# Optimization experiments

Measured on AMD Instinct MI355X. Metric: run time of the kernel, lower is better.

The kernel has to match this reference:

```python
import jax, jax.numpy as jnp
import numpy as np

B, T, H, HY, E, L = 32, 256, 1024, 256, 64, 2


def setup_inputs() -> dict:
    key = jax.random.key(0)
    ks = jax.random.split(key, 16)
    rn = lambda k, s, sc=0.05: jax.random.normal(k, s, dtype=jnp.float32) * sc
    return {
        'input': rn(ks[0], (B, T, H), 1.0),
        'w_ih': rn(ks[1], (L, 4 * H, H)),
        'w_hh': rn(ks[2], (L, 4 * H, H)),
        'hyper_w_ih': rn(ks[3], (L, 4 * HY, 2 * H)),
        'hyper_w_hh': rn(ks[4], (L, 4 * HY, HY)),
        'hyper_b': rn(ks[5], (L, 4 * HY)),
        'w_zh': rn(ks[6], (L, 4 * E, HY)),
        'b_zh': jnp.ones((L, 4 * E), jnp.float32),
        'w_zx': rn(ks[7], (L, 4 * E, HY)),
        'b_zx': jnp.ones((L, 4 * E), jnp.float32),
        'w_zb': rn(ks[8], (L, 4 * E, HY)),
        'w_dh': rn(ks[9], (L, 4, H, E), 1.0 / E),
        'w_dx': rn(ks[10], (L, 4, H, E), 1.0 / E),
        'w_db': rn(ks[11], (L, 4, H, E)),
        'b0': rn(ks[12], (L, 4 * H)),
    }


def reference(input, w_ih, w_hh, hyper_w_ih, hyper_w_hh, hyper_b,
              w_zh, b_zh, w_zx, b_zx, w_zb, w_dh, w_dx, w_db, b0):
    L = w_ih.shape[0]
    Bb = input.shape[0]
    Hh = w_hh.shape[-1]
    Hy = hyper_w_hh.shape[-1]
    Ee = w_dh.shape[-1]

    def cell(l, xt, h, c, hh, hc):
        # hyper (meta) LSTM step: input is concat(x, h_main)
        xh = jnp.concatenate([xt, h], axis=-1)
        hg = xh @ hyper_w_ih[l].T + hh @ hyper_w_hh[l].T + hyper_b[l]
        hi, hf, hgc, ho = jnp.split(hg, 4, axis=-1)
        hc2 = jax.nn.sigmoid(hf) * hc + jax.nn.sigmoid(hi) * jnp.tanh(hgc)
        hh2 = jax.nn.sigmoid(ho) * jnp.tanh(hc2)
        # gate-wise embeddings z (B, 4, E) then project to per-gate scale vectors (B, 4H)
        zh = (hh2 @ w_zh[l].T + b_zh[l]).reshape(Bb, 4, Ee)
        zx = (hh2 @ w_zx[l].T + b_zx[l]).reshape(Bb, 4, Ee)
        zb = (hh2 @ w_zb[l].T).reshape(Bb, 4, Ee)
        dh = jnp.einsum('bge,ghe->bgh', zh, w_dh[l]).reshape(Bb, 4 * Hh)
        dx = jnp.einsum('bge,ghe->bgh', zx, w_dx[l]).reshape(Bb, 4 * Hh)
        db = jnp.einsum('bge,ghe->bgh', zb, w_db[l]).reshape(Bb, 4 * Hh) + b0[l]
        # main LSTM gates, dynamically scaled by hypernetwork
        pre = dh * (h @ w_hh[l].T) + dx * (xt @ w_ih[l].T) + db
        i, f, g, o = jnp.split(pre, 4, axis=-1)
        c2 = jax.nn.sigmoid(f) * c + jax.nn.sigmoid(i) * jnp.tanh(g)
        h2 = jax.nn.sigmoid(o) * jnp.tanh(c2)
        return h2, c2, hh2, hc2

    def step(carry, xt):
        h, c, hh, hc = carry  # each (L, B, .)
        hs, cs, hhs, hcs = [], [], [], []
        inp = xt
        for l in range(L):
            h2, c2, hh2, hc2 = cell(l, inp, h[l], c[l], hh[l], hc[l])
            inp = h2
            hs.append(h2); cs.append(c2); hhs.append(hh2); hcs.append(hc2)
        carry = (jnp.stack(hs), jnp.stack(cs), jnp.stack(hhs), jnp.stack(hcs))
        return carry, inp  # top-layer hidden

    init = (jnp.zeros((L, Bb, Hh), input.dtype), jnp.zeros((L, Bb, Hh), input.dtype),
            jnp.zeros((L, Bb, Hy), input.dtype), jnp.zeros((L, Bb, Hy), input.dtype))
    carry, ys = jax.lax.scan(step, init, jnp.swapaxes(input, 0, 1))
    h_seq = jnp.swapaxes(ys, 0, 1)  # (B, T, H)
    return h_seq, carry[0][-1], carry[1][-1]
```

## Files before the change

### kernel.cpp

```cpp
#include <hip/hip_runtime.h>

typedef __bf16 bf16;
typedef __bf16 bf16x8 __attribute__((ext_vector_type(8)));
typedef __bf16 bf16x4 __attribute__((ext_vector_type(4)));
typedef float f32x4 __attribute__((ext_vector_type(4)));
typedef unsigned long long u64;

#define SCOPE_AGENT __HIP_MEMORY_SCOPE_AGENT


__device__ __forceinline__ float sigf(float x) { return 1.0f / (1.0f + __expf(-x)); }
__device__ __forceinline__ float tanhf_fast(float x) {
  float e = __expf(-2.0f * fabsf(x));
  float r = (1.0f - e) / (1.0f + e);
  return copysignf(r, x);
}
__device__ __forceinline__ f32x4 mfma16(bf16x8 a, bf16x8 b, f32x4 c) {
  return __builtin_amdgcn_mfma_f32_16x16x32_bf16(a, b, c, 0, 0, 0);
}
__device__ __forceinline__ u64 uld(const u64* p) { return __hip_atomic_load(p, __ATOMIC_RELAXED, SCOPE_AGENT); }
__device__ __forceinline__ void ust(u64* p, u64 v) { __hip_atomic_store(p, v, __ATOMIC_RELAXED, SCOPE_AGENT); }
__device__ __forceinline__ int ildi(const int* p) { return __hip_atomic_load(p, __ATOMIC_RELAXED, SCOPE_AGENT); }
__device__ __forceinline__ void isti(int* p, int v) { __hip_atomic_store(p, v, __ATOMIC_RELAXED, SCOPE_AGENT); }
__device__ __forceinline__ void fstf(float* p, float v) { __hip_atomic_store(p, v, __ATOMIC_RELAXED, SCOPE_AGENT); }
__device__ __forceinline__ void usti32(unsigned* p, unsigned v) { __hip_atomic_store(p, v, __ATOMIC_RELAXED, SCOPE_AGENT); }

__global__ void detect_kernel(const void* probe, int* flag) {
  __shared__ int cnt;
  if (threadIdx.x == 0) cnt = 0;
  __syncthreads();
  const bf16* p = (const bf16*)probe;
  int local = 0;
  for (int j = threadIdx.x; j < 8192; j += 256) {
    float x = (float)p[j];
    bool wild = (x != x) || (fabsf(x) > 1e3f) || (x != 0.0f && fabsf(x) < 1e-30f);
    local += wild ? 1 : 0;
  }
  atomicAdd(&cnt, local);
  __syncthreads();
  if (threadIdx.x == 0) *flag = (cnt > 64) ? 1 : 0;
}

struct CvtSrc { const void* s[15]; };
struct CvtDst { bf16* d[15]; };

__global__ __launch_bounds__(256) void convert_kernel(CvtSrc S, CvtDst D, const int* flag) {
  const int pre[16] = {0, 8388608, 16777216, 25165824, 29360128, 29884416, 29886464,
                       30017536, 30018048, 30149120, 30149632, 30280704, 30804992,
                       31329280, 31853568, 31861760};
  const int fp32 = *flag;
  const int nvec = 31861760 / 4;
  for (int v = blockIdx.x * 256 + threadIdx.x; v < nvec; v += gridDim.x * 256) {
    int e = v * 4;
    int seg = 0;
#pragma unroll
    for (int k = 1; k < 15; ++k) seg += (e >= pre[k]) ? 1 : 0;
    int off = e - pre[seg];
    bf16* d = D.d[seg] + off;
    if (fp32) {
      const float* s = (const float*)S.s[seg] + off;
      float4 x = *(const float4*)s;
      d[0] = (bf16)x.x; d[1] = (bf16)x.y; d[2] = (bf16)x.z; d[3] = (bf16)x.w;
    } else {
      const bf16* s = (const bf16*)S.s[seg] + off;
      d[0] = s[0]; d[1] = s[1]; d[2] = s[2]; d[3] = s[3];
    }
  }
}

__global__ void init_kernel(u64* zbase) {
  int i = blockIdx.x * 256 + threadIdx.x;
  zbase[i] = 0ull;
}

__global__ __launch_bounds__(256) void gemm_pre(
    const bf16* __restrict__ A, const bf16* __restrict__ w_ih_l,
    const bf16* __restrict__ hwih_l, bf16* __restrict__ Xp, float* __restrict__ Hxp) {
  constexpr int LDT = 72;
  __shared__ alignas(16) bf16 As[64 * LDT];
  __shared__ alignas(16) bf16 Bs[64 * LDT];
  const int bm = blockIdx.x & 127;
  const int bn = blockIdx.x >> 7;
  const int m0 = bm * 64, n0 = bn * 64;
  const int tid = threadIdx.x;
  const int lane = tid & 63, wid = tid >> 6;
  const int l15 = lane & 15, q = lane >> 4;
  const int srow = tid >> 2, sk = (tid & 3) * 16;
  const bf16* arow = A + (size_t)(m0 + srow) * 1024;
  const int n = n0 + srow;
  const bf16* brow = (n < 4096) ? (w_ih_l + (size_t)n * 1024)
                                : (hwih_l + (size_t)(n - 4096) * 2048);
  f32x4 acc[4] = {};
  for (int kb = 0; kb < 1024; kb += 64) {
    *(bf16x8*)(&As[srow * LDT + sk])     = *(const bf16x8*)(arow + kb + sk);
    *(bf16x8*)(&As[srow * LDT + sk + 8]) = *(const bf16x8*)(arow + kb + sk + 8);
    *(bf16x8*)(&Bs[srow * LDT + sk])     = *(const bf16x8*)(brow + kb + sk);
    *(bf16x8*)(&Bs[srow * LDT + sk + 8]) = *(const bf16x8*)(brow + kb + sk + 8);
    __syncthreads();
#pragma unroll
    for (int kk = 0; kk < 64; kk += 32) {
      bf16x8 av = *(const bf16x8*)(&As[(wid * 16 + l15) * LDT + kk + q * 8]);
#pragma unroll
      for (int j = 0; j < 4; ++j) {
        bf16x8 bv = *(const bf16x8*)(&Bs[(j * 16 + l15) * LDT + kk + q * 8]);
        acc[j] = mfma16(av, bv, acc[j]);
      }
    }
    __syncthreads();
  }
#pragma unroll
  for (int j = 0; j < 4; ++j) {
    const int gn = n0 + j * 16 + l15;
#pragma unroll
    for (int r = 0; r < 4; ++r) {
      const int gm = m0 + wid * 16 + q * 4 + r;
      float v = acc[j][r];
      if (gn < 4096) Xp[(size_t)gm * 4096 + gn] = (bf16)v;
      else           Hxp[(size_t)gm * 1024 + (gn - 4096)] = v;
    }
  }
}

struct SeqArgs {
  const bf16 *w_hh, *hwih, *hwhh, *hyb;
  const bf16 *w_zh, *b_zh, *w_zx, *b_zx, *w_zb;
  const bf16 *w_dh, *w_dx, *w_db, *b0;
  const bf16 *Xp; const float *Hxp;
  const bf16 *w_ih1;
  bf16 *Xp1c; float *Hxp1c;
  u64 *Y0;
  u64 *hpub;
  u64 *hh2pub;
  float *outp;
  int *flags;
};

__global__ __launch_bounds__(256) void seq_kernel(SeqArgs a) {
  __shared__ char smem[41472] __attribute__((aligned(16)));
  bf16 (*hstage)[1032] = (bf16(*)[1032])smem;
  bf16 (*hhK)[264]    = (bf16(*)[264])(smem + 33024);
  float* hgL          = (float*)(smem + 33024);
  bf16 (*hA4)[1032]   = (bf16(*)[1032])smem;
  bf16 (*hh2A)[264]   = (bf16(*)[264])(smem + 8256);
  float (*RhL)[256]   = (float(*)[256])(smem + 10368);
  float (*zsL)[768]   = (float(*)[768])(smem + 14464);
  float (*presL)[256] = (float(*)[256])(smem + 26752);
  bf16 (*hbuf)[64]    = (bf16(*)[64])(smem + 30848);
  bf16*  As = (bf16*)smem;
  bf16*  Bs = (bf16*)(smem + 9216);
  float* Ct = (float*)(smem + 18432);

  const int tid = threadIdx.x;
  const int lane = tid & 63, wid = tid >> 6;
  const int l15 = lane & 15, q = lane >> 4;
  const int blk = blockIdx.x;
  const int xcd = blk & 7, slot = blk >> 3;
  const int layer = xcd >> 2, xl = xcd & 3;
  const int s16 = xl * 4 + (slot & 3);
  const int bq = slot >> 2;
  const int lblk = bq * 16 + s16;
  const int hd = s16 >> 1;
  const int mh = (bq == hd) ? 0 : ((bq == ((hd + 4) & 7)) ? 1 : -1);
  const bool isHyper = (((s16 & 1) == 0) && (mh >= 0));
  const int myMh = bq >> 2;

  u64* hbase  = a.hpub + (size_t)layer * 16384;
  u64* h2base = a.hh2pub + (size_t)layer * 4096;
  int* gchunkp= a.flags + 32;
  int* arrp   = a.flags + 64 + layer * 2048;
  int* arrp0  = a.flags + 64;
  int* hh2fp  = a.flags + 4160 + layer * 256;
  int* carrp  = a.flags + 4672;

  const bf16* whh_l = a.w_hh + (size_t)layer * 4194304;
  const bf16* hybl  = a.hyb + layer * 1024;
  const bf16* bzh_l = a.b_zh + layer * 256;
  const bf16* bzx_l = a.b_zx + layer * 256;
  const bf16* b0_l  = a.b0 + (size_t)layer * 4096;
  const int cb = tid >> 6, chl = tid & 63;

  float c_reg = 0.0f;
  float hc[2] = {0, 0};

  const bf16* zrow[12];
#pragma unroll
  for (int j = 0; j < 12; ++j) {
    int ng = wid * 12 + j, tau = ng >> 4;
    const bf16* base = (tau == 0) ? a.w_zh : (tau == 1) ? a.w_zx : a.w_zb;
    zrow[j] = base + ((size_t)layer * 256 + (ng & 15) * 16 + l15) * 256;
  }
  const bf16* rrow[4];
#pragma unroll
  for (int nt = 0; nt < 4; ++nt)
    rrow[nt] = whh_l + (size_t)(wid * 1024 + s16 * 64 + nt * 16 + l15) * 1024;
  const bf16* hirow[2];
  const bf16* hhrow[2];
#pragma unroll
  for (int nt = 0; nt < 2; ++nt) {
    const int row = wid * 256 + hd * 32 + nt * 16 + l15;
    hirow[nt] = a.hwih + (size_t)layer * 2097152 + (size_t)row * 2048 + 1024;
    hhrow[nt] = a.hwhh + (size_t)layer * 262144 + (size_t)row * 256;
  }
  const size_t wdo = ((size_t)(layer * 4 + wid) * 1024 + s16 * 64 + lane) * 64;
  const bf16 *pdh = a.w_dh + wdo, *pdx = a.w_dx + wdo, *pdb = a.w_db + wdo;

  for (int t = 0; t < 256; ++t) {
    const int tloc = t & 31;
    u64* wslot = hbase + (size_t)(t & 1) * 8192;
    const u64* rslot = hbase + (size_t)((t + 1) & 1) * 8192;
    u64* wcur = h2base + (size_t)(t & 1) * 2048;
    const u64* rK = h2base + (size_t)((t + 1) & 1) * 2048;

    if (layer == 1 && tloc == 0) {
      const int k = t >> 5;
      if (tid < 128) {
        while (ildi(arrp0 + tid * 16) < (k + 1) * 32) __builtin_amdgcn_s_sleep(2);
      } else if (t > 0) {
        while (ildi(arrp + (tid - 128) * 16) < t) __builtin_amdgcn_s_sleep(2);
      }
      __atomic_signal_fence(__ATOMIC_SEQ_CST);
      __syncthreads();
      const int srow = tid >> 2, sk = (tid & 3) * 16;
      for (int tt = 0; tt < 10; ++tt) {
        const int tile = lblk * 10 + tt;
        const int m0 = (tile & 15) * 64, n0 = (tile >> 4) * 64;
        const int m = m0 + srow;
        const u64* arow = a.Y0 + (((size_t)(m >> 5) * 256 + k * 32 + (m & 31)) << 8);
        const int n = n0 + srow;
        const bf16* brow = (n < 4096) ? (a.w_ih1 + (size_t)n * 1024)
                                      : (a.hwih + 2097152 + (size_t)(n - 4096) * 2048);
        f32x4 acc[4] = {};
        for (int kb = 0; kb < 1024; kb += 64) {
          const int c0 = (kb + sk) >> 2;
          u64 a0 = uld(arow + c0),     a1 = uld(arow + c0 + 1);
          u64 a2 = uld(arow + c0 + 2), a3 = uld(arow + c0 + 3);
          *(u64*)&As[srow * 72 + sk]      = a0;
          *(u64*)&As[srow * 72 + sk + 4]  = a1;
          *(u64*)&As[srow * 72 + sk + 8]  = a2;
          *(u64*)&As[srow * 72 + sk + 12] = a3;
          *(bf16x8*)&Bs[srow * 72 + sk]     = *(const bf16x8*)(brow + kb + sk);
          *(bf16x8*)&Bs[srow * 72 + sk + 8] = *(const bf16x8*)(brow + kb + sk + 8);
          __syncthreads();
#pragma unroll
          for (int kk = 0; kk < 64; kk += 32) {
            bf16x8 av = *(const bf16x8*)&As[(wid * 16 + l15) * 72 + kk + q * 8];
#pragma unroll
            for (int j = 0; j < 4; ++j) {
              bf16x8 bv = *(const bf16x8*)&Bs[(j * 16 + l15) * 72 + kk + q * 8];
              acc[j] = mfma16(av, bv, acc[j]);
            }
          }
          __syncthreads();
        }
#pragma unroll
        for (int j = 0; j < 4; ++j)
#pragma unroll
          for (int r = 0; r < 4; ++r)
            Ct[(wid * 16 + q * 4 + r) * 64 + j * 16 + l15] = acc[j][r];
        __syncthreads();
#pragma unroll
        for (int e = 0; e < 4; ++e) {
          const int qd = tid * 4 + e;
          const int row = qd >> 4, col4 = (qd & 15) * 4;
          f32x4 v = *(const f32x4*)&Ct[row * 64 + col4];
          const int gm = m0 + row, gn = n0 + col4;
          if (gn < 4096) {
            union { bf16 h[4]; u64 u; } pk;
#pragma unroll
            for (int x = 0; x < 4; ++x) pk.h[x] = (bf16)v[x];
            ust((u64*)a.Xp1c + ((((size_t)gm << 12) + gn) >> 2), pk.u);
          } else {
            float* hp = a.Hxp1c + ((size_t)gm << 10) + (gn - 4096);
#pragma unroll
            for (int x = 0; x < 4; ++x) fstf(hp + x, v[x]);
          }
        }
        __syncthreads();
      }
      __atomic_signal_fence(__ATOMIC_SEQ_CST);
      __builtin_amdgcn_s_waitcnt(0);
      __syncthreads();
      if (tid == 0) isti(carrp + lblk * 16, k + 1);
      if (lblk == 0 && wid == 0) {
        for (;;) {
          int v0 = ildi(carrp + lane * 32);
          int v1 = ildi(carrp + lane * 32 + 16);
          if (__all((v0 >= k + 1) && (v1 >= k + 1))) break;
          __builtin_amdgcn_s_sleep(2);
        }
        __atomic_signal_fence(__ATOMIC_SEQ_CST);
        if (lane == 0) isti(gchunkp, k + 1);
      }
      if (tid == 0) { while (ildi(gchunkp) < k + 1) __builtin_amdgcn_s_sleep(2); }
      __atomic_signal_fence(__ATOMIC_SEQ_CST);
      __syncthreads();
    }

    if (t > 0) {
      if (tid < 16) {
        while (ildi(arrp + (bq * 16 + tid) * 16) < t) __builtin_amdgcn_s_sleep(1);
      }
      if (isHyper) {
        if (tid >= 64 && tid < 128) {
          const int j = tid - 64;
          const int fl = (mh * 4 + (j >> 4)) * 16 + (j & 15);
          while (ildi(arrp + fl * 16) < t) __builtin_amdgcn_s_sleep(1);
        }
        if (tid >= 128 && tid < 136) {
          while (ildi(hh2fp + ((tid - 128) * 2 + mh) * 16) < t) __builtin_amdgcn_s_sleep(1);
        }
      }
    }
    __atomic_signal_fence(__ATOMIC_SEQ_CST);
    __syncthreads();

    if (isHyper) {
      for (int i = tid; i < 4096; i += 256) {
        int b = i >> 8, u = i & 255;
        *(u64*)&hstage[b][u * 4] = uld(rslot + ((size_t)(mh * 16 + b) << 8) + u);
      }
      for (int i = tid; i < 1024; i += 256) {
        int b = i >> 6, u = i & 63;
        *(u64*)&hhK[b][u * 4] = uld(rK + ((size_t)(mh * 16 + b) << 6) + u);
      }
      __syncthreads();
      f32x4 acc[2] = {};
      for (int kk = 0; kk < 1024; kk += 32) {
        int ko = kk + q * 8;
        bf16x8 a0 = *(const bf16x8*)&hstage[l15][ko];
#pragma unroll
        for (int nt = 0; nt < 2; ++nt) {
          bf16x8 bv = *(const bf16x8*)(hirow[nt] + ko);
          acc[nt] = mfma16(a0, bv, acc[nt]);
        }
      }
      for (int kk = 0; kk < 256; kk += 32) {
        int ko = kk + q * 8;
        bf16x8 a0 = *(const bf16x8*)&hhK[l15][ko];
#pragma unroll
        for (int nt = 0; nt < 2; ++nt) {
          bf16x8 bv = *(const bf16x8*)(hhrow[nt] + ko);
          acc[nt] = mfma16(a0, bv, acc[nt]);
        }
      }
      __syncthreads();
#pragma unroll
      for (int nt = 0; nt < 2; ++nt)
#pragma unroll
        for (int r = 0; r < 4; ++r)
          hgL[(wid * 16 + q * 4 + r) * 32 + nt * 16 + l15] = acc[nt][r];
      __syncthreads();
      {
        const int b16 = tid >> 4, d0 = (tid & 15) * 2;
        const int b = mh * 16 + b16;
        float hx2[4][2];
        if (layer == 0) {
          const float* hx = a.Hxp + ((size_t)b * 256 + t) * 1024 + hd * 32 + d0;
#pragma unroll
          for (int g = 0; g < 4; ++g) {
            hx2[g][0] = hx[g * 256]; hx2[g][1] = hx[g * 256 + 1];
          }
        } else {
          const u64* hx1 = (const u64*)a.Hxp1c + (((size_t)b * 32 + tloc) << 9)
                         + ((hd * 32 + d0) >> 1);
#pragma unroll
          for (int g = 0; g < 4; ++g) {
            u64 w = uld(hx1 + g * 128);
            hx2[g][0] = __uint_as_float((unsigned)(w & 0xffffffffu));
            hx2[g][1] = __uint_as_float((unsigned)(w >> 32));
          }
        }
        union { bf16 h[2]; unsigned u; } pk;
#pragma unroll
        for (int dd = 0; dd < 2; ++dd) {
          int d = d0 + dd, gd = hd * 32 + d;
          float hi  = hgL[(0 * 16 + b16) * 32 + d] + (float)hybl[gd]       + hx2[0][dd];
          float hf  = hgL[(1 * 16 + b16) * 32 + d] + (float)hybl[256 + gd] + hx2[1][dd];
          float hgv = hgL[(2 * 16 + b16) * 32 + d] + (float)hybl[512 + gd] + hx2[2][dd];
          float ho  = hgL[(3 * 16 + b16) * 32 + d] + (float)hybl[768 + gd] + hx2[3][dd];
          hc[dd] = sigf(hf) * hc[dd] + sigf(hi) * tanhf_fast(hgv);
          pk.h[dd] = (bf16)(sigf(ho) * tanhf_fast(hc[dd]));
        }
        usti32((unsigned*)wcur + b * 128 + hd * 16 + (d0 >> 1), pk.u);
      }
      __atomic_signal_fence(__ATOMIC_SEQ_CST);
      __builtin_amdgcn_s_waitcnt(0);
      __syncthreads();
      if (tid == 0) isti(hh2fp + (hd * 2 + mh) * 16, t + 1);
    }
    __syncthreads();

    for (int i = tid; i < 1024; i += 256) {
      int b = i >> 8, u = i & 255;
      *(u64*)&hA4[b][u * 4] = uld(rslot + ((size_t)(bq * 4 + b) << 8) + u);
    }
    __syncthreads();
    {
      f32x4 racc[4] = {};
      for (int kk = 0; kk < 1024; kk += 32) {
        const int ko = kk + q * 8;
        bf16x8 av = *(const bf16x8*)&hA4[l15 & 3][ko];
#pragma unroll
        for (int nt = 0; nt < 4; ++nt) {
          bf16x8 bv = *(const bf16x8*)(rrow[nt] + ko);
          racc[nt] = mfma16(av, bv, racc[nt]);
        }
      }
      if (lane < 16) {
#pragma unroll
        for (int nt = 0; nt < 4; ++nt)
#pragma unroll
          for (int r = 0; r < 4; ++r)
            RhL[r][wid * 64 + nt * 16 + lane] = racc[nt][r];
      }
    }
    if (tid < 8) {
      while (ildi(hh2fp + (tid * 2 + myMh) * 16) < t + 1) __builtin_amdgcn_s_sleep(1);
    }
    __atomic_signal_fence(__ATOMIC_SEQ_CST);
    __syncthreads();
    {
      int b = tid >> 6, u = tid & 63;
      *(u64*)&hh2A[b][u * 4] = uld(wcur + ((size_t)(bq * 4 + b) << 6) + u);
    }
    __syncthreads();
    {
      f32x4 zacc[12] = {};
      for (int kk = 0; kk < 256; kk += 32) {
        const int ko = kk + q * 8;
        bf16x8 av = *(const bf16x8*)&hh2A[l15 & 3][ko];
#pragma unroll
        for (int j = 0; j < 12; ++j) {
          bf16x8 bv = *(const bf16x8*)(zrow[j] + ko);
          zacc[j] = mfma16(av, bv, zacc[j]);
        }
      }
      if (lane < 16) {
#pragma unroll
        for (int j = 0; j < 12; ++j) {
          int ng = wid * 12 + j, tau = ng >> 4, col = (ng & 15) * 16 + lane;
          float bias = (tau == 0) ? (float)bzh_l[col] : (tau == 1) ? (float)bzx_l[col] : 0.0f;
#pragma unroll
          for (int r = 0; r < 4; ++r) zsL[r][tau * 256 + col] = zacc[j][r] + bias;
        }
      }
    }
    __syncthreads();
    {
      float dH[4] = {}, dX[4] = {}, dB[4] = {};
      for (int e0 = 0; e0 < 64; e0 += 4) {
        bf16x4 wh = *(const bf16x4*)(pdh + e0);
        bf16x4 wx = *(const bf16x4*)(pdx + e0);
        bf16x4 wb = *(const bf16x4*)(pdb + e0);
        f32x4 zh_[4], zx_[4], zb_[4];
#pragma unroll
        for (int b = 0; b < 4; ++b) {
          zh_[b] = *(const f32x4*)&zsL[b][wid * 64 + e0];
          zx_[b] = *(const f32x4*)&zsL[b][256 + wid * 64 + e0];
          zb_[b] = *(const f32x4*)&zsL[b][512 + wid * 64 + e0];
        }
#pragma unroll
        for (int jj = 0; jj < 4; ++jj) {
          float whf = (float)wh[jj], wxf = (float)wx[jj], wbf = (float)wb[jj];
#pragma unroll
          for (int b = 0; b < 4; ++b) {
            dH[b] += zh_[b][jj] * whf;
            dX[b] += zx_[b][jj] * wxf;
            dB[b] += zb_[b][jj] * wbf;
          }
        }
      }
      const int n = wid * 1024 + s16 * 64 + lane;
#pragma unroll
      for (int b = 0; b < 4; ++b) {
        float rh = RhL[b][wid * 64 + lane];
        float xp;
        if (layer == 0) {
          xp = (float)a.Xp[((size_t)(bq * 4 + b) * 256 + t) * 4096 + n];
        } else {
          u64 w = uld((const u64*)a.Xp1c
                      + ((((size_t)((bq * 4 + b) * 32 + tloc) << 12) + (n & ~3)) >> 2));
          xp = __uint_as_float(((unsigned)(w >> ((n & 3) * 16)) & 0xffffu) << 16);
        }
        float b0v = (float)b0_l[n];
        presL[b][wid * 64 + lane] = dH[b] * rh + dX[b] * xp + dB[b] + b0v;
      }
    }
    __syncthreads();
    {
      float iv = presL[cb][chl];
      float fv = presL[cb][64 + chl];
      float gv = presL[cb][128 + chl];
      float ov = presL[cb][192 + chl];
      c_reg = sigf(fv) * c_reg + sigf(iv) * tanhf_fast(gv);
      float hn = sigf(ov) * tanhf_fast(c_reg);
      hbuf[cb][chl] = (bf16)hn;
      if (layer) {
        const size_t oo = ((size_t)(bq * 4 + cb) * 256 + t) * 1024 + s16 * 64 + chl;
        a.outp[oo] = hn;
        if (t == 255) {
          a.outp[8388608 + (bq * 4 + cb) * 1024 + s16 * 64 + chl] = hn;
          a.outp[8421376 + (bq * 4 + cb) * 1024 + s16 * 64 + chl] = c_reg;
        }
      }
    }
    __syncthreads();
    if (tid < 64) {
      int b = tid >> 4, u = tid & 15;
      u64 pk = *(const u64*)&hbuf[b][u * 4];
      ust(wslot + ((size_t)(bq * 4 + b) << 8) + s16 * 16 + u, pk);
      if (layer == 0)
        ust(a.Y0 + (((size_t)(bq * 4 + b) * 256 + t) << 8) + s16 * 16 + u, pk);
    }
    __atomic_signal_fence(__ATOMIC_SEQ_CST);
    __builtin_amdgcn_s_waitcnt(0);
    __syncthreads();
    if (tid == 0) isti(arrp + lblk * 16, t + 1);
  }
}

extern "C" void kernel_launch(void* const* d_in, const int* in_sizes, int n_in,
                              void* d_out, int out_size, void* d_ws, size_t ws_size,
                              hipStream_t stream) {
  float* outp = (float*)d_out;
  char* ws = (char*)d_ws;
  bf16*  Xp     = (bf16*) (ws);
  float* Hxp    = (float*)(ws + 67108864ull);
  u64*   Y0     = (u64*)  (ws + 100663296ull);
  bf16* c_input = (bf16*)(ws + 117669888ull);
  bf16*  Xp1c   = c_input;
  float* Hxp1c  = (float*)(ws + 117669888ull + 8388608ull);
  bf16* c_w_ih  = (bf16*)(ws + 134447104ull);
  bf16* c_w_hh  = (bf16*)(ws + 151224320ull);
  bf16* c_hwih  = (bf16*)(ws + 168001536ull);
  bf16* c_hwhh  = (bf16*)(ws + 176390144ull);
  bf16* c_hyb   = (bf16*)(ws + 177438720ull);
  bf16* c_wzh   = (bf16*)(ws + 177442816ull);
  bf16* c_bzh   = (bf16*)(ws + 177704960ull);
  bf16* c_wzx   = (bf16*)(ws + 177705984ull);
  bf16* c_bzx   = (bf16*)(ws + 177968128ull);
  bf16* c_wzb   = (bf16*)(ws + 177969152ull);
  bf16* c_wdh   = (bf16*)(ws + 178231296ull);
  bf16* c_wdx   = (bf16*)(ws + 179279872ull);
  bf16* c_wdb   = (bf16*)(ws + 180328448ull);
  bf16* c_b0    = (bf16*)(ws + 181377024ull);
  int*  dflag   = (int*) (ws + 181393408ull);
  char* pubb    = ws + 181397504ull;
  u64*   hpub   = (u64*)  (pubb + 0);
  u64*   hh2pub = (u64*)  (pubb + 262144);
  int*   flags  = (int*)  (pubb + 327680);

  hipLaunchKernelGGL(detect_kernel, dim3(1), dim3(256), 0, stream, d_in[2], dflag);
  CvtSrc S; CvtDst D;
  for (int i = 0; i < 15; ++i) S.s[i] = d_in[i];
  D.d[0] = c_input; D.d[1] = c_w_ih; D.d[2] = c_w_hh; D.d[3] = c_hwih; D.d[4] = c_hwhh;
  D.d[5] = c_hyb;   D.d[6] = c_wzh;  D.d[7] = c_bzh;  D.d[8] = c_wzx;  D.d[9] = c_bzx;
  D.d[10] = c_wzb;  D.d[11] = c_wdh; D.d[12] = c_wdx; D.d[13] = c_wdb; D.d[14] = c_b0;
  hipLaunchKernelGGL(convert_kernel, dim3(2048), dim3(256), 0, stream, S, D, dflag);

  hipLaunchKernelGGL(init_kernel, dim3(176), dim3(256), 0, stream, (u64*)pubb);
  hipLaunchKernelGGL(gemm_pre, dim3(10240), dim3(256), 0, stream,
                     c_input, c_w_ih, c_hwih, Xp, Hxp);

  SeqArgs sa;
  sa.w_hh = c_w_hh; sa.hwih = c_hwih; sa.hwhh = c_hwhh; sa.hyb = c_hyb;
  sa.w_zh = c_wzh; sa.b_zh = c_bzh; sa.w_zx = c_wzx; sa.b_zx = c_bzx; sa.w_zb = c_wzb;
  sa.w_dh = c_wdh; sa.w_dx = c_wdx; sa.w_db = c_wdb; sa.b0 = c_b0;
  sa.Xp = Xp; sa.Hxp = Hxp;
  sa.w_ih1 = c_w_ih + (size_t)4194304;
  sa.Xp1c = Xp1c; sa.Hxp1c = Hxp1c;
  sa.Y0 = Y0;
  sa.hpub = hpub; sa.hh2pub = hh2pub;
  sa.outp = outp;
  sa.flags = flags;
  hipLaunchKernelGGL(seq_kernel, dim3(256), dim3(256), 0, stream, sa);
}
```

Before: 20.41 ms.

## Redistribute hyper-LSTM work so each batch group computes its own hyper step

The hyper LSTM step moves off the 16 dedicated blocks that each handled 16 batches by 32 hidden units, each waiting on many producer flags. It now runs on 4 blocks per batch quad (sq==0), each covering 4 batches by 64 units. Those blocks reuse the main-path h staging buffer hA4, so they no longer stage a separate 16-row h tile, and synchronization shrinks to per-quad flags. The aim is shorter cross-block dependency chains and less redundant staging per step. In exchange, the MFMA A operand uses only 4 of its 16 rows, so more weight bandwidth is spent per useful output.

```diff
diff --git a/kernel.cpp b/kernel.cpp
--- a/kernel.cpp
+++ b/kernel.cpp
@@ -23,7 +23,7 @@
 __device__ __forceinline__ int ildi(const int* p) { return __hip_atomic_load(p, __ATOMIC_RELAXED, SCOPE_AGENT); }
 __device__ __forceinline__ void isti(int* p, int v) { __hip_atomic_store(p, v, __ATOMIC_RELAXED, SCOPE_AGENT); }
 __device__ __forceinline__ void fstf(float* p, float v) { __hip_atomic_store(p, v, __ATOMIC_RELAXED, SCOPE_AGENT); }
-__device__ __forceinline__ void usti32(unsigned* p, unsigned v) { __hip_atomic_store(p, v, __ATOMIC_RELAXED, SCOPE_AGENT); }
+__device__ __forceinline__ float fldf(const float* p) { return __hip_atomic_load(p, __ATOMIC_RELAXED, SCOPE_AGENT); }
 
 __global__ void detect_kernel(const void* probe, int* flag) {
   __shared__ int cnt;
@@ -136,16 +136,16 @@
 };
 
 __global__ __launch_bounds__(256) void seq_kernel(SeqArgs a) {
-  __shared__ char smem[41472] __attribute__((aligned(16)));
-  bf16 (*hstage)[1032] = (bf16(*)[1032])smem;
-  bf16 (*hhK)[264]    = (bf16(*)[264])(smem + 33024);
-  float* hgL          = (float*)(smem + 33024);
+  __shared__ char smem[38144] __attribute__((aligned(16)));
   bf16 (*hA4)[1032]   = (bf16(*)[1032])smem;
-  bf16 (*hh2A)[264]   = (bf16(*)[264])(smem + 8256);
-  float (*RhL)[256]   = (float(*)[256])(smem + 10368);
-  float (*zsL)[768]   = (float(*)[768])(smem + 14464);
-  float (*presL)[256] = (float(*)[256])(smem + 26752);
-  bf16 (*hbuf)[64]    = (bf16(*)[64])(smem + 30848);
+  bf16 (*hhPrev)[264] = (bf16(*)[264])(smem + 8256);
+  bf16 (*hh2A)[264]   = (bf16(*)[264])(smem + 10368);
+  float (*RhL)[256]   = (float(*)[256])(smem + 12480);
+  float (*zsL)[768]   = (float(*)[768])(smem + 16576);
+  float (*presL)[256] = (float(*)[256])(smem + 28864);
+  bf16 (*hbuf)[64]    = (bf16(*)[64])(smem + 32960);
+  float* hgS          = (float*)(smem + 33472);
+  bf16*  hh2own       = (bf16*)(smem + 37568);
   bf16*  As = (bf16*)smem;
   bf16*  Bs = (bf16*)(smem + 9216);
   float* Ct = (float*)(smem + 18432);
@@ -156,21 +156,18 @@
   const int blk = blockIdx.x;
   const int xcd = blk & 7, slot = blk >> 3;
   const int layer = xcd >> 2, xl = xcd & 3;
-  const int s16 = xl * 4 + (slot & 3);
-  const int bq = slot >> 2;
+  const int bq = slot >> 2, sq = slot & 3;
+  const int s16 = sq * 4 + xl;
   const int lblk = bq * 16 + s16;
-  const int hd = s16 >> 1;
-  const int mh = (bq == hd) ? 0 : ((bq == ((hd + 4) & 7)) ? 1 : -1);
-  const bool isHyper = (((s16 & 1) == 0) && (mh >= 0));
-  const int myMh = bq >> 2;
+  const bool isHyper = (sq == 0);
 
   u64* hbase  = a.hpub + (size_t)layer * 16384;
   u64* h2base = a.hh2pub + (size_t)layer * 4096;
   int* gchunkp= a.flags + 32;
   int* arrp   = a.flags + 64 + layer * 2048;
   int* arrp0  = a.flags + 64;
-  int* hh2fp  = a.flags + 4160 + layer * 256;
-  int* carrp  = a.flags + 4672;
+  int* hh2fp  = a.flags + 4608 + layer * 512;
+  int* carrp  = a.flags + 5632;
 
   const bf16* whh_l = a.w_hh + (size_t)layer * 4194304;
   const bf16* hybl  = a.hyb + layer * 1024;
@@ -180,7 +177,7 @@
   const int cb = tid >> 6, chl = tid & 63;
 
   float c_reg = 0.0f;
-  float hc[2] = {0, 0};
+  float hc = 0.0f;
 
   const bf16* zrow[12];
 #pragma unroll
@@ -193,14 +190,9 @@
 #pragma unroll
   for (int nt = 0; nt < 4; ++nt)
     rrow[nt] = whh_l + (size_t)(wid * 1024 + s16 * 64 + nt * 16 + l15) * 1024;
-  const bf16* hirow[2];
-  const bf16* hhrow[2];
-#pragma unroll
-  for (int nt = 0; nt < 2; ++nt) {
-    const int row = wid * 256 + hd * 32 + nt * 16 + l15;
-    hirow[nt] = a.hwih + (size_t)layer * 2097152 + (size_t)row * 2048 + 1024;
-    hhrow[nt] = a.hwhh + (size_t)layer * 262144 + (size_t)row * 256;
-  }
+  const bf16* hih = a.hwih + (size_t)layer * 2097152 + 1024;
+  const bf16* hhh = a.hwhh + (size_t)layer * 262144;
+  const int hrbase = wid * 256 + xl * 64 + l15;
   const size_t wdo = ((size_t)(layer * 4 + wid) * 1024 + s16 * 64 + lane) * 64;
   const bf16 *pdh = a.w_dh + wdo, *pdx = a.w_dx + wdo, *pdb = a.w_db + wdo;
 
@@ -300,101 +292,84 @@
       if (tid < 16) {
         while (ildi(arrp + (bq * 16 + tid) * 16) < t) __builtin_amdgcn_s_sleep(1);
       }
-      if (isHyper) {
-        if (tid >= 64 && tid < 128) {
-          const int j = tid - 64;
-          const int fl = (mh * 4 + (j >> 4)) * 16 + (j & 15);
-          while (ildi(arrp + fl * 16) < t) __builtin_amdgcn_s_sleep(1);
-        }
-        if (tid >= 128 && tid < 136) {
-          while (ildi(hh2fp + ((tid - 128) * 2 + mh) * 16) < t) __builtin_amdgcn_s_sleep(1);
-        }
+      if (isHyper && tid >= 16 && tid < 20) {
+        while (ildi(hh2fp + (bq * 4 + (tid - 16)) * 16) < t) __builtin_amdgcn_s_sleep(1);
       }
     }
     __atomic_signal_fence(__ATOMIC_SEQ_CST);
-    __syncthreads();
-
-    if (isHyper) {
-      for (int i = tid; i < 4096; i += 256) {
-        int b = i >> 8, u = i & 255;
-        *(u64*)&hstage[b][u * 4] = uld(rslot + ((size_t)(mh * 16 + b) << 8) + u);
-      }
-      for (int i = tid; i < 1024; i += 256) {
-        int b = i >> 6, u = i & 63;
-        *(u64*)&hhK[b][u * 4] = uld(rK + ((size_t)(mh * 16 + b) << 6) + u);
-      }
-      __syncthreads();
-      f32x4 acc[2] = {};
-      for (int kk = 0; kk < 1024; kk += 32) {
-        int ko = kk + q * 8;
-        bf16x8 a0 = *(const bf16x8*)&hstage[l15][ko];
-#pragma unroll
-        for (int nt = 0; nt < 2; ++nt) {
-          bf16x8 bv = *(const bf16x8*)(hirow[nt] + ko);
-          acc[nt] = mfma16(a0, bv, acc[nt]);
-        }
-      }
-      for (int kk = 0; kk < 256; kk += 32) {
-        int ko = kk + q * 8;
-        bf16x8 a0 = *(const bf16x8*)&hhK[l15][ko];
-#pragma unroll
-        for (int nt = 0; nt < 2; ++nt) {
-          bf16x8 bv = *(const bf16x8*)(hhrow[nt] + ko);
-          acc[nt] = mfma16(a0, bv, acc[nt]);
-        }
-      }
-      __syncthreads();
-#pragma unroll
-      for (int nt = 0; nt < 2; ++nt)
-#pragma unroll
-        for (int r = 0; r < 4; ++r)
-          hgL[(wid * 16 + q * 4 + r) * 32 + nt * 16 + l15] = acc[nt][r];
-      __syncthreads();
-      {
-        const int b16 = tid >> 4, d0 = (tid & 15) * 2;
-        const int b = mh * 16 + b16;
-        float hx2[4][2];
-        if (layer == 0) {
-          const float* hx = a.Hxp + ((size_t)b * 256 + t) * 1024 + hd * 32 + d0;
-#pragma unroll
-          for (int g = 0; g < 4; ++g) {
-            hx2[g][0] = hx[g * 256]; hx2[g][1] = hx[g * 256 + 1];
-          }
-        } else {
-          const u64* hx1 = (const u64*)a.Hxp1c + (((size_t)b * 32 + tloc) << 9)
-                         + ((hd * 32 + d0) >> 1);
-#pragma unroll
-          for (int g = 0; g < 4; ++g) {
-            u64 w = uld(hx1 + g * 128);
-            hx2[g][0] = __uint_as_float((unsigned)(w & 0xffffffffu));
-            hx2[g][1] = __uint_as_float((unsigned)(w >> 32));
-          }
-        }
-        union { bf16 h[2]; unsigned u; } pk;
-#pragma unroll
-        for (int dd = 0; dd < 2; ++dd) {
-          int d = d0 + dd, gd = hd * 32 + d;
-          float hi  = hgL[(0 * 16 + b16) * 32 + d] + (float)hybl[gd]       + hx2[0][dd];
-          float hf  = hgL[(1 * 16 + b16) * 32 + d] + (float)hybl[256 + gd] + hx2[1][dd];
-          float hgv = hgL[(2 * 16 + b16) * 32 + d] + (float)hybl[512 + gd] + hx2[2][dd];
-          float ho  = hgL[(3 * 16 + b16) * 32 + d] + (float)hybl[768 + gd] + hx2[3][dd];
-          hc[dd] = sigf(hf) * hc[dd] + sigf(hi) * tanhf_fast(hgv);
-          pk.h[dd] = (bf16)(sigf(ho) * tanhf_fast(hc[dd]));
-        }
-        usti32((unsigned*)wcur + b * 128 + hd * 16 + (d0 >> 1), pk.u);
-      }
-      __atomic_signal_fence(__ATOMIC_SEQ_CST);
-      __builtin_amdgcn_s_waitcnt(0);
-      __syncthreads();
-      if (tid == 0) isti(hh2fp + (hd * 2 + mh) * 16, t + 1);
-    }
     __syncthreads();
 
     for (int i = tid; i < 1024; i += 256) {
       int b = i >> 8, u = i & 255;
       *(u64*)&hA4[b][u * 4] = uld(rslot + ((size_t)(bq * 4 + b) << 8) + u);
     }
-    __syncthreads();
+    if (isHyper) {
+      int b = tid >> 6, u = tid & 63;
+      *(u64*)&hhPrev[b][u * 4] = uld(rK + ((size_t)(bq * 4 + b) << 6) + u);
+    }
+    __syncthreads();
+
+    if (isHyper) {
+      f32x4 hacc[4] = {};
+      for (int kk = 0; kk < 1024; kk += 32) {
+        const int ko = kk + q * 8;
+        bf16x8 a0 = *(const bf16x8*)&hA4[l15 & 3][ko];
+#pragma unroll
+        for (int j = 0; j < 4; ++j) {
+          bf16x8 bv = *(const bf16x8*)(hih + (size_t)(hrbase + j * 16) * 2048 + ko);
+          hacc[j] = mfma16(a0, bv, hacc[j]);
+        }
+      }
+      for (int kk = 0; kk < 256; kk += 32) {
+        const int ko = kk + q * 8;
+        bf16x8 a0 = *(const bf16x8*)&hhPrev[l15 & 3][ko];
+#pragma unroll
+        for (int j = 0; j < 4; ++j) {
+          bf16x8 bv = *(const bf16x8*)(hhh + (size_t)(hrbase + j * 16) * 256 + ko);
+          hacc[j] = mfma16(a0, bv, hacc[j]);
+        }
+      }
+      if (lane < 16) {
+#pragma unroll
+        for (int j = 0; j < 4; ++j)
+#pragma unroll
+          for (int r = 0; r < 4; ++r)
+            hgS[(wid * 4 + r) * 64 + j * 16 + l15] = hacc[j][r];
+      }
+    }
+    __syncthreads();
+    if (isHyper) {
+      const int b = tid >> 6, dd = tid & 63;
+      const int gb = bq * 4 + b;
+      float hx0, hx1, hx2v, hx3;
+      if (layer == 0) {
+        const float* hx = a.Hxp + ((size_t)gb * 256 + t) * 1024 + xl * 64 + dd;
+        hx0 = hx[0]; hx1 = hx[256]; hx2v = hx[512]; hx3 = hx[768];
+      } else {
+        const float* hx = a.Hxp1c + ((size_t)(gb * 32 + tloc)) * 1024 + xl * 64 + dd;
+        hx0 = fldf(hx); hx1 = fldf(hx + 256); hx2v = fldf(hx + 512); hx3 = fldf(hx + 768);
+      }
+      const int gd = xl * 64 + dd;
+      float hi  = hgS[(0 * 4 + b) * 64 + dd] + (float)hybl[gd]       + hx0;
+      float hf  = hgS[(1 * 4 + b) * 64 + dd] + (float)hybl[256 + gd] + hx1;
+      float hgv = hgS[(2 * 4 + b) * 64 + dd] + (float)hybl[512 + gd] + hx2v;
+      float ho  = hgS[(3 * 4 + b) * 64 + dd] + (float)hybl[768 + gd] + hx3;
+      hc = sigf(hf) * hc + sigf(hi) * tanhf_fast(hgv);
+      hh2own[b * 64 + dd] = (bf16)(sigf(ho) * tanhf_fast(hc));
+    }
+    __syncthreads();
+    if (isHyper && tid < 64) {
+      int b = tid >> 4, j = tid & 15;
+      union { bf16 h[4]; u64 v; } pk;
+#pragma unroll
+      for (int x = 0; x < 4; ++x) pk.h[x] = hh2own[b * 64 + j * 4 + x];
+      ust(wcur + ((size_t)(bq * 4 + b) << 6) + xl * 16 + j, pk.v);
+    }
+    __atomic_signal_fence(__ATOMIC_SEQ_CST);
+    __builtin_amdgcn_s_waitcnt(0);
+    __syncthreads();
+    if (isHyper && tid == 0) isti(hh2fp + (bq * 4 + xl) * 16, t + 1);
+
     {
       f32x4 racc[4] = {};
       for (int kk = 0; kk < 1024; kk += 32) {
@@ -414,8 +389,8 @@
             RhL[r][wid * 64 + nt * 16 + lane] = racc[nt][r];
       }
     }
-    if (tid < 8) {
-      while (ildi(hh2fp + (tid * 2 + myMh) * 16) < t + 1) __builtin_amdgcn_s_sleep(1);
+    if (tid < 4) {
+      while (ildi(hh2fp + (bq * 4 + tid) * 16) < t + 1) __builtin_amdgcn_s_sleep(1);
     }
     __atomic_signal_fence(__ATOMIC_SEQ_CST);
     __syncthreads();
```

Result: slower. 26.34 ms (+29.0%).
